# Optimization experiments

Measured on AMD Instinct MI355X. Metric: run time of the kernel, lower is better.

## Reference

```python
import jax, jax.numpy as jnp
import numpy as np

N_NODES = 100000
N_EDGES = 1600000


def setup_inputs() -> dict:
    key = jax.random.key(0)
    k1, k2, k3, k4, k5 = jax.random.split(key, 5)
    node_states = jax.random.normal(k1, (N_NODES, 128), dtype=jnp.float32)
    edge_index = jax.random.randint(k2, (2, N_EDGES), 0, N_NODES, dtype=jnp.int64)
    mask = jax.random.uniform(k3, (N_EDGES,), dtype=jnp.float32)  # edge weights
    # Glorot-ish init for the two GCN linear layers
    W1 = jax.random.normal(k4, (128, 64), dtype=jnp.float32) * 0.05
    b1 = jnp.zeros((64,), dtype=jnp.float32)
    W2 = jax.random.normal(k5, (64, 64), dtype=jnp.float32) * 0.05
    b2 = jnp.zeros((64,), dtype=jnp.float32)
    return {"node_states": node_states, "edge_index": edge_index, "mask": mask,
            "W1": W1, "b1": b1, "W2": W2, "b2": b2}


def _gcn_layer(x, src, dst, edge_w, W, b, n_nodes):
    # PyG GCNConv (normalize=False): h = x @ W; out[dst] += edge_w * h[src]; out += b
    h = x @ W                                  # [N, d_out]
    msg = h[src] * edge_w[:, None]             # [E, d_out] gather + scale
    agg = jax.ops.segment_sum(msg, dst, num_segments=n_nodes)  # scatter-add
    return agg + b


def reference(node_states, edge_index, mask, W1, b1, W2, b2):
    src = edge_index[0]
    dst = edge_index[1]
    n = node_states.shape[0]
    h1 = jax.nn.relu(_gcn_layer(node_states, src, dst, mask, W1, b1, n))
    h2 = jax.nn.relu(_gcn_layer(h1, src, dst, mask, W2, b2, n))
    return h2
```

## Files before the change

### kernel.cpp

```cpp
#include <hip/hip_runtime.h>
#include <hip/hip_bf16.h>

#define N_NODES 100000
#define N_EDGES 1600000
#define NB_C 391
#define NB_F 1563
#define NBLK_S 391
#define CHUNK_E 4096
#define CAPC 4608
#define QCAP 1280
#define GCSTRIDE 32
#define FIXSCALE 1048576.0f
#define FIXINV   (1.0f / 1048576.0f)


typedef short v8s __attribute__((ext_vector_type(8)));
typedef float v4f __attribute__((ext_vector_type(4)));

static __device__ __forceinline__ unsigned pack_bf2(float a, float b) {
    __hip_bfloat162 p = __float22bfloat162_rn(make_float2(a, b));
    return *reinterpret_cast<unsigned*>(&p);
}
static __device__ __forceinline__ float2 bf2_to_f2(unsigned u) {
    __hip_bfloat162 p = *reinterpret_cast<__hip_bfloat162*>(&u);
    return __bfloat1622float2(p);
}

__global__ __launch_bounds__(1024) void k1_sort_gemm(const int* __restrict__ src,
                                                     const int* __restrict__ dst,
                                                     const float* __restrict__ wgt,
                                                     const float* __restrict__ x,
                                                     const float* __restrict__ W1,
                                                     int* __restrict__ gcount,
                                                     int2* __restrict__ arena,
                                                     unsigned* __restrict__ hpre) {
    __shared__ __align__(16) int smem[13976];
    const int b = blockIdx.x;
    const int t = threadIdx.x;

    if (b >= NBLK_S) {
        unsigned* xs = (unsigned*)smem;
        unsigned* ws = (unsigned*)smem + 64 * 68;
        const int tile = b - NBLK_S;
        const int row0 = tile * 64;
        {
            const float2* g2 = (const float2*)W1;
            for (int i = t; i < 64 * 128 / 2; i += 1024) {
                const float2 v = g2[i];
                const int k = (2 * i) >> 6;
                const int c = (2 * i) & 63;
                ((short*)&ws[c * 68])[k]       = (short)(pack_bf2(v.x, 0.f) & 0xFFFF);
                ((short*)&ws[(c + 1) * 68])[k] = (short)(pack_bf2(v.y, 0.f) & 0xFFFF);
            }
        }
        {
            const float4* g = (const float4*)x;
            for (int i = t; i < 64 * 32; i += 1024) {
                const int r = i >> 5, cu = i & 31;
                const int row = row0 + r;
                uint2 v = make_uint2(0u, 0u);
                if (row < N_NODES) {
                    float4 f = g[(size_t)row * 32 + cu];
                    v.x = pack_bf2(f.x, f.y);
                    v.y = pack_bf2(f.z, f.w);
                }
                *(uint2*)&xs[r * 68 + 2 * cu] = v;
            }
        }
        __syncthreads();
        const int w = t >> 6, lane = t & 63;
        const int l15 = lane & 15, quad = lane >> 4;
        const int a  = w & 3;
        const int g_ = w >> 2;
        v4f acc = (v4f){0.f, 0.f, 0.f, 0.f};
#pragma unroll
        for (int k0 = 0; k0 < 128; k0 += 32) {
            const int ku = k0 / 2 + quad * 4;
            const v8s xb = *(const v8s*)&xs[(g_ * 16 + l15) * 68 + ku];
            const v8s wa = *(const v8s*)&ws[(16 * a + l15) * 68 + ku];
            acc = __builtin_amdgcn_mfma_f32_16x16x32_bf16(wa, xb, acc, 0, 0, 0);
        }
        __syncthreads();
        float* stg = (float*)smem;
        *(v4f*)&stg[(g_ * 16 + l15) * 68 + 16 * a + 4 * quad] = acc;
        __syncthreads();
        for (int i2 = t; i2 < 2048; i2 += 1024) {
            const int nl = i2 >> 5, d = i2 & 31;
            const int row = row0 + nl;
            if (row < N_NODES)
                hpre[(size_t)row * 32 + d] = pack_bf2(stg[nl * 68 + d], stg[nl * 68 + d + 32]);
        }
        return;
    }

    int*  hist  = smem;
    int*  lcur  = smem + 391;
    int*  tgb   = smem + 782;
    int*  pairs = smem + 1173;
    int*  tg    = smem + 1685;
    int2* ord   = (int2*)(smem + 5782);

    for (int i = t; i < NB_C; i += 1024) hist[i] = 0;
    __syncthreads();

    const int e0 = b * CHUNK_E;
    const int n = min(CHUNK_E, N_EDGES - e0);
    const int nI4 = n >> 2;
    const bool act = t < nI4;
    int4 sv, dv; float4 wv;
    if (act) {
        sv = ((const int4*)(src + e0))[t];
        dv = ((const int4*)(dst + e0))[t];
        wv = ((const float4*)(wgt + e0))[t];
        atomicAdd(&hist[dv.x >> 8], 1);
        atomicAdd(&hist[dv.y >> 8], 1);
        atomicAdd(&hist[dv.z >> 8], 1);
        atomicAdd(&hist[dv.w >> 8], 1);
    }
    __syncthreads();
    if (t < 512) pairs[t] = (t < NB_C) ? hist[t] : 0;
    __syncthreads();
    for (int off = 1; off < 512; off <<= 1) {
        int u = 0;
        if (t < 512 && t >= off) u = pairs[t - off];
        __syncthreads();
        if (t < 512) pairs[t] += u;
        __syncthreads();
    }
    if (t < NB_C) lcur[t] = pairs[t] - hist[t];
    __syncthreads();
    for (int i = t; i < NB_C; i += 1024) {
        const int hv = hist[i];
        const int lb = lcur[i];
        const int grsv = (hv > 0) ? atomicAdd(&gcount[i * GCSTRIDE], hv) : 0;
        tgb[i] = i * CAPC + grsv - lb;
    }
    __syncthreads();
    if (act) {
        {
            const int bk = dv.x >> 8;
            const int lp = atomicAdd(&lcur[bk], 1);
            ord[lp] = make_int2(sv.x | ((dv.x & 255) << 17), __float_as_int(wv.x));
            tg[lp] = tgb[bk] + lp;
        }
        {
            const int bk = dv.y >> 8;
            const int lp = atomicAdd(&lcur[bk], 1);
            ord[lp] = make_int2(sv.y | ((dv.y & 255) << 17), __float_as_int(wv.y));
            tg[lp] = tgb[bk] + lp;
        }
        {
            const int bk = dv.z >> 8;
            const int lp = atomicAdd(&lcur[bk], 1);
            ord[lp] = make_int2(sv.z | ((dv.z & 255) << 17), __float_as_int(wv.z));
            tg[lp] = tgb[bk] + lp;
        }
        {
            const int bk = dv.w >> 8;
            const int lp = atomicAdd(&lcur[bk], 1);
            ord[lp] = make_int2(sv.w | ((dv.w & 255) << 17), __float_as_int(wv.w));
            tg[lp] = tgb[bk] + lp;
        }
    }
    __syncthreads();
    for (int i = t; i < n; i += 1024)
        arena[tg[i]] = ord[i];
}

template<bool FUSE>
__global__ __launch_bounds__(256) void gather_fuse(const unsigned* __restrict__ hsrc,
                                                   const int2* __restrict__ arena,
                                                   const int* __restrict__ gcount,
                                                   const float* __restrict__ bias,
                                                   const float* __restrict__ W2,
                                                   void* __restrict__ outp) {
    __shared__ int accs[64 * 68];
    __shared__ int2 qrec[QCAP];
    __shared__ int qn_s;
    extern __shared__ unsigned wsdyn[];
    const int t = threadIdx.x;

    const int orig = blockIdx.x;
    const int xcd = orig & 7, idx = orig >> 3;
    const int b = (xcd < 3 ? xcd * 196 : 3 * 196 + (xcd - 3) * 195) + idx;

    const int cb = b >> 2;
    const int sub = b & 3;
    for (int i = t; i < 4096; i += 256) accs[i] = 0;
    if (t == 0) qn_s = 0;
    if constexpr (FUSE) {
        const float2* g2 = (const float2*)W2;
        for (int i = t; i < 2048; i += 256) {
            const float2 v = g2[i];
            const int k = (2 * i) >> 6;
            const int c = (2 * i) & 63;
            ((short*)&wsdyn[c * 36])[k]       = (short)(pack_bf2(v.x, 0.f) & 0xFFFF);
            ((short*)&wsdyn[(c + 1) * 36])[k] = (short)(pack_bf2(v.y, 0.f) & 0xFFFF);
        }
    }
    __syncthreads();

    const int cntc = min(gcount[cb * GCSTRIDE], CAPC);
    const size_t cbase = (size_t)cb * CAPC;
    for (int i = t; i < cntc; i += 256) {
        const int2 r = arena[cbase + i];
        if (((r.x >> 23) & 3) == sub) {
            const int pos = atomicAdd(&qn_s, 1);
            if (pos < QCAP) qrec[pos] = r;
        }
    }
    __syncthreads();
    const int qn = min(qn_s, QCAP);
    const int npad = (qn + 127) & ~127;
    for (int i = qn + t; i < npad; i += 256) qrec[i] = make_int2(0, 0);
    __syncthreads();

    const int li2 = t & 15;
    const int s   = t >> 4;
    const int qw  = s & 3;
    const int da  = (li2 + 8 * qw) & 31;
    const int db  = (da + 16) & 31;
    for (int ib = s; ib < npad; ib += 128) {
        int2 r[8];
#pragma unroll
        for (int j = 0; j < 8; ++j) r[j] = qrec[ib + 16 * j];
        unsigned ha[8], hb[8];
#pragma unroll
        for (int j = 0; j < 8; ++j) {
            const unsigned* row = hsrc + (size_t)(r[j].x & 0x1FFFF) * 32;
            ha[j] = row[da];
            hb[j] = row[db];
        }
#pragma unroll
        for (int j = 0; j < 8; ++j) {
            const int dl = (r[j].x >> 17) & 63;
            const float wsf = __int_as_float(r[j].y) * FIXSCALE;
            const float2 fa = bf2_to_f2(ha[j]);
            const float2 fb = bf2_to_f2(hb[j]);
            atomicAdd(&accs[dl * 64 + da],      (int)(wsf * fa.x));
            atomicAdd(&accs[dl * 64 + da + 32], (int)(wsf * fa.y));
            atomicAdd(&accs[dl * 64 + db],      (int)(wsf * fb.x));
            atomicAdd(&accs[dl * 64 + db + 32], (int)(wsf * fb.y));
        }
    }
    __syncthreads();

    const int lane = t & 63;
    if constexpr (FUSE) {
        unsigned pk[8];
#pragma unroll
        for (int k = 0; k < 8; ++k) {
            const int i2 = t + k * 256;
            const int node = i2 >> 5, cp = i2 & 31;
            const float f0 = fmaxf((float)accs[node * 64 + 2 * cp]     * FIXINV + bias[2 * cp],     0.f);
            const float f1 = fmaxf((float)accs[node * 64 + 2 * cp + 1] * FIXINV + bias[2 * cp + 1], 0.f);
            pk[k] = pack_bf2(f0, f1);
        }
        __syncthreads();
        unsigned* xs = (unsigned*)accs;
#pragma unroll
        for (int k = 0; k < 8; ++k) {
            const int i2 = t + k * 256;
            const int node = i2 >> 5, cp = i2 & 31;
            xs[node * 36 + cp] = pk[k];
        }
        __syncthreads();
        const int w = t >> 6, l15 = lane & 15, quad = lane >> 4;
        v4f a4[4];
#pragma unroll
        for (int tt = 0; tt < 4; ++tt) a4[tt] = (v4f){0.f, 0.f, 0.f, 0.f};
#pragma unroll
        for (int k0 = 0; k0 < 64; k0 += 32) {
            const int ku = k0 / 2 + quad * 4;
            const v8s xb = *(const v8s*)&xs[(w * 16 + l15) * 36 + ku];
#pragma unroll
            for (int tt = 0; tt < 4; ++tt) {
                const v8s wa = *(const v8s*)&wsdyn[(16 * tt + l15) * 36 + ku];
                a4[tt] = __builtin_amdgcn_mfma_f32_16x16x32_bf16(wa, xb, a4[tt], 0, 0, 0);
            }
        }
        __syncthreads();
        float* stg = (float*)accs;
#pragma unroll
        for (int tt = 0; tt < 4; ++tt)
            *(v4f*)&stg[(w * 16 + l15) * 68 + 16 * tt + 4 * quad] = a4[tt];
        __syncthreads();
        for (int i2 = t; i2 < 2048; i2 += 256) {
            const int nl = i2 >> 5, d = i2 & 31;
            const int ng = b * 64 + nl;
            if (ng < N_NODES)
                ((unsigned*)outp)[(size_t)ng * 32 + d] =
                    pack_bf2(stg[nl * 68 + d], stg[nl * 68 + d + 32]);
        }
    } else {
        for (int i2 = t; i2 < 2048; i2 += 256) {
            const int node = i2 >> 5, cp = i2 & 31;
            const int ng = b * 64 + node;
            if (ng < N_NODES) {
                float2 o;
                o.x = fmaxf((float)accs[node * 64 + 2 * cp]     * FIXINV + bias[2 * cp],     0.f);
                o.y = fmaxf((float)accs[node * 64 + 2 * cp + 1] * FIXINV + bias[2 * cp + 1], 0.f);
                *(float2*)&((float*)outp)[(size_t)ng * 64 + 2 * cp] = o;
            }
        }
    }
}

extern "C" void kernel_launch(void* const* d_in, const int* in_sizes, int n_in,
                              void* d_out, int out_size, void* d_ws, size_t ws_size,
                              hipStream_t stream) {
    const float* x    = (const float*)d_in[0];
    const int*   eidx = (const int*)d_in[1];
    const float* mask = (const float*)d_in[2];
    const float* W1   = (const float*)d_in[3];
    const float* b1   = (const float*)d_in[4];
    const float* W2   = (const float*)d_in[5];
    const float* b2   = (const float*)d_in[6];
    float* out = (float*)d_out;

    const int* src = eidx;
    const int* dst = eidx + N_EDGES;

    unsigned* hpre = (unsigned*)d_out;

    int2*     arena  = (int2*)d_ws;
    int*      gcount = (int*)(arena + (size_t)NB_C * CAPC);
    unsigned* hpre2  = (unsigned*)(gcount + NB_C * GCSTRIDE);

    const int gemmBlocks = (N_NODES + 63) / 64;

    hipMemsetAsync(gcount, 0, NB_C * GCSTRIDE * sizeof(int), stream);

    k1_sort_gemm<<<NBLK_S + gemmBlocks, 1024, 0, stream>>>(src, dst, mask, x, W1,
                                                           gcount, arena, hpre);

    gather_fuse<true><<<NB_F, 256, 64 * 36 * 4, stream>>>(hpre, arena, gcount,
                                                          b1, W2, hpre2);
    gather_fuse<false><<<NB_F, 256, 0, stream>>>(hpre2, arena, gcount,
                                                 b2, nullptr, out);
}
```

Measured before the change: 221.6 us.

## Halve gather block tile to 32 nodes with ballot-compacted queue and wider loads

The gather/aggregate kernel now handles 32 destination nodes per block instead of 64, doubling the block count and splitting each coarse bucket into 8 sub-buckets instead of 4. Queue fill uses a wave ballot plus popcount so there is one LDS atomic per wave, not one per edge. Feature reads become single 8-byte loads per edge with a lane-rotated atomic pattern to spread LDS bank conflicts. The fused MFMA epilogue is reshaped for the smaller tile. This adds parallelism and cuts LDS use, at the cost of rescanning each bucket's arena records 8 times and dropping the bounds checks on output nodes.

```diff
diff --git a/kernel.cpp b/kernel.cpp
--- a/kernel.cpp
+++ b/kernel.cpp
@@ -4,11 +4,11 @@
 #define N_NODES 100000
 #define N_EDGES 1600000
 #define NB_C 391
-#define NB_F 1563
+#define NB_F 3125
 #define NBLK_S 391
 #define CHUNK_E 4096
 #define CAPC 4608
-#define QCAP 1280
+#define QCAP 768
 #define GCSTRIDE 32
 #define FIXSCALE 1048576.0f
 #define FIXINV   (1.0f / 1048576.0f)
@@ -174,7 +174,7 @@
                                                    const float* __restrict__ bias,
                                                    const float* __restrict__ W2,
                                                    void* __restrict__ outp) {
-    __shared__ int accs[64 * 68];
+    __shared__ int accs[32 * 68];
     __shared__ int2 qrec[QCAP];
     __shared__ int qn_s;
     extern __shared__ unsigned wsdyn[];
@@ -182,11 +182,11 @@
 
     const int orig = blockIdx.x;
     const int xcd = orig & 7, idx = orig >> 3;
-    const int b = (xcd < 3 ? xcd * 196 : 3 * 196 + (xcd - 3) * 195) + idx;
-
-    const int cb = b >> 2;
-    const int sub = b & 3;
-    for (int i = t; i < 4096; i += 256) accs[i] = 0;
+    const int b = (xcd < 5 ? xcd * 391 : 5 * 391 + (xcd - 5) * 390) + idx;
+
+    const int cb = b >> 3;
+    const int sub = b & 7;
+    for (int i = t; i < 2048; i += 256) accs[i] = 0;
     if (t == 0) qn_s = 0;
     if constexpr (FUSE) {
         const float2* g2 = (const float2*)W2;
@@ -200,56 +200,67 @@
     }
     __syncthreads();
 
-    const int cntc = min(gcount[cb * GCSTRIDE], CAPC);
-    const size_t cbase = (size_t)cb * CAPC;
-    for (int i = t; i < cntc; i += 256) {
-        const int2 r = arena[cbase + i];
-        if (((r.x >> 23) & 3) == sub) {
-            const int pos = atomicAdd(&qn_s, 1);
-            if (pos < QCAP) qrec[pos] = r;
+    const int lane = t & 63;
+    {
+        const int cntc = min(gcount[cb * GCSTRIDE], CAPC);
+        const size_t cbase = (size_t)cb * CAPC;
+        const unsigned long long below = (lane == 63) ? ~0ull >> 1
+                                                      : (1ull << lane) - 1;
+        for (int i = t; i < cntc; i += 256) {
+            const int2 r = arena[cbase + i];
+            const bool keep = ((r.x >> 22) & 7) == sub;
+            const unsigned long long m = __ballot(keep);
+            int base = 0;
+            if (lane == 0) base = atomicAdd(&qn_s, __popcll(m));
+            base = __builtin_amdgcn_readfirstlane(base);
+            if (keep) {
+                const int pos = base + __popcll(m & below);
+                if (pos < QCAP) qrec[pos] = r;
+            }
         }
     }
     __syncthreads();
     const int qn = min(qn_s, QCAP);
-    const int npad = (qn + 127) & ~127;
+    const int npad = (qn + 63) & ~63;
     for (int i = qn + t; i < npad; i += 256) qrec[i] = make_int2(0, 0);
     __syncthreads();
 
     const int li2 = t & 15;
     const int s   = t >> 4;
     const int qw  = s & 3;
-    const int da  = (li2 + 8 * qw) & 31;
-    const int db  = (da + 16) & 31;
-    for (int ib = s; ib < npad; ib += 128) {
-        int2 r[8];
-#pragma unroll
-        for (int j = 0; j < 8; ++j) r[j] = qrec[ib + 16 * j];
-        unsigned ha[8], hb[8];
-#pragma unroll
-        for (int j = 0; j < 8; ++j) {
-            const unsigned* row = hsrc + (size_t)(r[j].x & 0x1FFFF) * 32;
-            ha[j] = row[da];
-            hb[j] = row[db];
-        }
-#pragma unroll
-        for (int j = 0; j < 8; ++j) {
-            const int dl = (r[j].x >> 17) & 63;
+    const int m   = (li2 + 4 * qw) & 15;
+    const int p   = qw & 1;
+    for (int ib = s; ib < npad; ib += 64) {
+        int2 r[4];
+#pragma unroll
+        for (int j = 0; j < 4; ++j) r[j] = qrec[ib + 16 * j];
+        uint2 hv[4];
+#pragma unroll
+        for (int j = 0; j < 4; ++j)
+            hv[j] = *(const uint2*)&hsrc[(size_t)(r[j].x & 0x1FFFF) * 32 + 2 * m];
+#pragma unroll
+        for (int j = 0; j < 4; ++j) {
+            const int dl = (r[j].x >> 17) & 31;
             const float wsf = __int_as_float(r[j].y) * FIXSCALE;
-            const float2 fa = bf2_to_f2(ha[j]);
-            const float2 fb = bf2_to_f2(hb[j]);
-            atomicAdd(&accs[dl * 64 + da],      (int)(wsf * fa.x));
-            atomicAdd(&accs[dl * 64 + da + 32], (int)(wsf * fa.y));
-            atomicAdd(&accs[dl * 64 + db],      (int)(wsf * fb.x));
-            atomicAdd(&accs[dl * 64 + db + 32], (int)(wsf * fb.y));
-        }
-    }
-    __syncthreads();
-
-    const int lane = t & 63;
+            const float2 fa = bf2_to_f2(hv[j].x);
+            const float2 fb = bf2_to_f2(hv[j].y);
+            int* ap = &accs[dl * 64 + 2 * m];
+            const float v0 = p ? fb.x : fa.x;
+            const float v1 = p ? fa.x : fb.x;
+            const float v2 = p ? fb.y : fa.y;
+            const float v3 = p ? fa.y : fb.y;
+            atomicAdd(ap + p,          (int)(wsf * v0));
+            atomicAdd(ap + 1 - p,      (int)(wsf * v1));
+            atomicAdd(ap + 32 + p,     (int)(wsf * v2));
+            atomicAdd(ap + 33 - p,     (int)(wsf * v3));
+        }
+    }
+    __syncthreads();
+
     if constexpr (FUSE) {
-        unsigned pk[8];
-#pragma unroll
-        for (int k = 0; k < 8; ++k) {
+        unsigned pk[4];
+#pragma unroll
+        for (int k = 0; k < 4; ++k) {
             const int i2 = t + k * 256;
             const int node = i2 >> 5, cp = i2 & 31;
             const float f0 = fmaxf((float)accs[node * 64 + 2 * cp]     * FIXINV + bias[2 * cp],     0.f);
@@ -259,49 +270,43 @@
         __syncthreads();
         unsigned* xs = (unsigned*)accs;
 #pragma unroll
-        for (int k = 0; k < 8; ++k) {
+        for (int k = 0; k < 4; ++k) {
             const int i2 = t + k * 256;
-            const int node = i2 >> 5, cp = i2 & 31;
-            xs[node * 36 + cp] = pk[k];
-        }
-        __syncthreads();
-        const int w = t >> 6, l15 = lane & 15, quad = lane >> 4;
-        v4f a4[4];
-#pragma unroll
-        for (int tt = 0; tt < 4; ++tt) a4[tt] = (v4f){0.f, 0.f, 0.f, 0.f};
+            xs[(i2 >> 5) * 36 + (i2 & 31)] = pk[k];
+        }
+        __syncthreads();
+        const int l15 = lane & 15, quad = lane >> 4;
+        const int w = t >> 6;
+        v4f a0 = (v4f){0.f, 0.f, 0.f, 0.f};
+        v4f a1 = (v4f){0.f, 0.f, 0.f, 0.f};
 #pragma unroll
         for (int k0 = 0; k0 < 64; k0 += 32) {
             const int ku = k0 / 2 + quad * 4;
-            const v8s xb = *(const v8s*)&xs[(w * 16 + l15) * 36 + ku];
-#pragma unroll
-            for (int tt = 0; tt < 4; ++tt) {
-                const v8s wa = *(const v8s*)&wsdyn[(16 * tt + l15) * 36 + ku];
-                a4[tt] = __builtin_amdgcn_mfma_f32_16x16x32_bf16(wa, xb, a4[tt], 0, 0, 0);
-            }
+            const v8s wa  = *(const v8s*)&wsdyn[(16 * w + l15) * 36 + ku];
+            const v8s xb0 = *(const v8s*)&xs[l15 * 36 + ku];
+            const v8s xb1 = *(const v8s*)&xs[(16 + l15) * 36 + ku];
+            a0 = __builtin_amdgcn_mfma_f32_16x16x32_bf16(wa, xb0, a0, 0, 0, 0);
+            a1 = __builtin_amdgcn_mfma_f32_16x16x32_bf16(wa, xb1, a1, 0, 0, 0);
         }
         __syncthreads();
         float* stg = (float*)accs;
-#pragma unroll
-        for (int tt = 0; tt < 4; ++tt)
-            *(v4f*)&stg[(w * 16 + l15) * 68 + 16 * tt + 4 * quad] = a4[tt];
-        __syncthreads();
-        for (int i2 = t; i2 < 2048; i2 += 256) {
+        *(v4f*)&stg[l15 * 68 + 16 * w + 4 * quad] = a0;
+        *(v4f*)&stg[(16 + l15) * 68 + 16 * w + 4 * quad] = a1;
+        __syncthreads();
+        for (int i2 = t; i2 < 1024; i2 += 256) {
             const int nl = i2 >> 5, d = i2 & 31;
-            const int ng = b * 64 + nl;
-            if (ng < N_NODES)
-                ((unsigned*)outp)[(size_t)ng * 32 + d] =
-                    pack_bf2(stg[nl * 68 + d], stg[nl * 68 + d + 32]);
+            const int ng = b * 32 + nl;
+            ((unsigned*)outp)[(size_t)ng * 32 + d] =
+                pack_bf2(stg[nl * 68 + d], stg[nl * 68 + d + 32]);
         }
     } else {
-        for (int i2 = t; i2 < 2048; i2 += 256) {
+        for (int i2 = t; i2 < 1024; i2 += 256) {
             const int node = i2 >> 5, cp = i2 & 31;
-            const int ng = b * 64 + node;
-            if (ng < N_NODES) {
-                float2 o;
-                o.x = fmaxf((float)accs[node * 64 + 2 * cp]     * FIXINV + bias[2 * cp],     0.f);
-                o.y = fmaxf((float)accs[node * 64 + 2 * cp + 1] * FIXINV + bias[2 * cp + 1], 0.f);
-                *(float2*)&((float*)outp)[(size_t)ng * 64 + 2 * cp] = o;
-            }
+            const int ng = b * 32 + node;
+            float2 o;
+            o.x = fmaxf((float)accs[node * 64 + 2 * cp]     * FIXINV + bias[2 * cp],     0.f);
+            o.y = fmaxf((float)accs[node * 64 + 2 * cp + 1] * FIXINV + bias[2 * cp + 1], 0.f);
+            *(float2*)&((float*)outp)[(size_t)ng * 64 + 2 * cp] = o;
         }
     }
 }
```

Result: slower. 227.1 us (+2.5%).
